# Performance work log

Measured on AMD Instinct MI355X. Metric: run time of the kernel, lower is better.

## Reference

```python
import jax, jax.numpy as jnp
import numpy as np

N, C_IN, C_OUT, T, V = 64, 128, 128, 128, 25
REL = C_IN // 8  # rel_channels = 16


def setup_inputs() -> dict:
    key = jax.random.key(0)
    ks = jax.random.split(key, 12)
    s_in = 1.0 / np.sqrt(C_IN)
    s_rel = 1.0 / np.sqrt(REL)
    return {
        "x": jax.random.normal(ks[0], (N, C_IN, T, V), jnp.float32),
        "A": jax.random.normal(ks[1], (V, V), jnp.float32),
        "alpha": jnp.float32(1.0),
        "W1": jax.random.normal(ks[2], (REL, C_IN), jnp.float32) * s_in,
        "b1": jnp.zeros((REL,), jnp.float32),
        "W2": jax.random.normal(ks[3], (REL, C_IN), jnp.float32) * s_in,
        "b2": jnp.zeros((REL,), jnp.float32),
        "W3": jax.random.normal(ks[4], (C_OUT, C_IN), jnp.float32) * s_in,
        "b3": jnp.zeros((C_OUT,), jnp.float32),
        "W4": jax.random.normal(ks[5], (C_OUT, REL), jnp.float32) * s_rel,
        "b4": jnp.zeros((C_OUT,), jnp.float32),
    }


def reference(x, A, alpha, W1, b1, W2, b2, W3, b3, W4, b4):
    # conv1(x).mean(-2) and conv2(x).mean(-2): 1x1 conv is linear, so mean over
    # T commutes with it -> compute mean first to avoid an (N,REL,T,V) temp.
    xm = x.mean(axis=2)                                        # (N, C, V)
    x1 = jnp.einsum('rc,ncv->nrv', W1, xm) + b1[None, :, None]  # (N, R, V)
    x2 = jnp.einsum('rc,ncv->nrv', W2, xm) + b2[None, :, None]  # (N, R, V)
    x3 = jnp.einsum('oc,nctv->notv', W3, x) + b3[None, :, None, None]  # (N,O,T,V)
    # tanh of broadcasted pairwise difference: (N, R, V, V)
    d = jnp.tanh(x1[:, :, :, None] - x2[:, :, None, :])
    # conv4 (1x1 over channel dim) -> learned per-channel adjacency
    adj = jnp.einsum('or,nrvu->novu', W4, d) + b4[None, :, None, None]
    adj = adj * alpha + A[None, None, :, :]                    # (N, O, V, V)
    return jnp.einsum('ncvu,nctv->nctu', adj, x3)              # (N, O, T, V)
```

## Files before the change

kernel.cpp:

```cpp
#include <hip/hip_runtime.h>


#define NB   64
#define CIN  128
#define COUT 128
#define TT   128
#define VV   25
#define REL  16

#define JT 25
#define KT 4
#define XF_BYTES (JT * KT * 1024)
#define X3_STRIDE 1040
#define LDS_BYTES (COUT * X3_STRIDE)

typedef __attribute__((ext_vector_type(8))) short bf16x8;
typedef __attribute__((ext_vector_type(4))) float f32x4;

__device__ inline short f2bf(float f) {
    unsigned u = __float_as_uint(f);
    u += 0x7fff + ((u >> 16) & 1);
    return (short)(u >> 16);
}

__launch_bounds__(256)
__global__ void k_mean(const float* __restrict__ x, float* __restrict__ xm) {
    __shared__ float tile[4 * 3200];
    int tid = threadIdx.x;
    int c0 = blockIdx.x * 4, n = blockIdx.y;
    const float* src = x + ((size_t)n * CIN + c0) * 3200;
    for (int i = tid; i < 3200; i += 256)
        *reinterpret_cast<float4*>(&tile[i * 4]) =
            *reinterpret_cast<const float4*>(src + (size_t)i * 4);
    __syncthreads();
    if (tid < 100) {
        int cl = tid / 25, v = tid - cl * 25;
        const float* r = &tile[cl * 3200 + v];
        float s = 0.f;
#pragma unroll
        for (int t = 0; t < TT; ++t) s += r[t * 25];
        xm[((size_t)n * CIN + c0 + cl) * 25 + v] = s * (1.0f / TT);
    }
}

__global__ void k_adj(const float* __restrict__ xm,
                      const float* __restrict__ A, const float* __restrict__ alphap,
                      const float* __restrict__ W1, const float* __restrict__ b1,
                      const float* __restrict__ W2, const float* __restrict__ b2,
                      const float* __restrict__ W4, const float* __restrict__ b4,
                      const float* __restrict__ W3, char* __restrict__ W3f,
                      char* __restrict__ adjT) {
    __shared__ char adjS[32 * 2048];
    __shared__ float xms[CIN * VV];
    __shared__ float W1s[REL * CIN];
    __shared__ float W2s[REL * CIN];
    __shared__ float x1s[REL * VV];
    __shared__ float x2s[REL * VV];
    __shared__ float W4s[32 * REL];
    __shared__ float b4s[32];

    int tid = threadIdx.x;
    int n = blockIdx.x;
    int o0 = blockIdx.y * 32;

    if (n == 0) {
#pragma unroll
        for (int pass = 0; pass < 2; ++pass) {
            int chunk = blockIdx.y * 512 + pass * 256 + tid;
            int l = chunk & 63;
            int frag = chunk >> 6;
            int ct = frag >> 2, kt = frag & 3;
            int c = ct * 16 + (l & 15);
            int kb = kt * 32 + 8 * (l >> 4);
            const float4 f0 = *reinterpret_cast<const float4*>(&W3[(size_t)c * CIN + kb]);
            const float4 f1 = *reinterpret_cast<const float4*>(&W3[(size_t)c * CIN + kb + 4]);
            bf16x8 vv;
            vv[0] = f2bf(f0.x); vv[1] = f2bf(f0.y); vv[2] = f2bf(f0.z); vv[3] = f2bf(f0.w);
            vv[4] = f2bf(f1.x); vv[5] = f2bf(f1.y); vv[6] = f2bf(f1.z); vv[7] = f2bf(f1.w);
            *reinterpret_cast<bf16x8*>(W3f + (size_t)chunk * 16) = vv;
        }
    }

    for (int i = tid; i < 16384; i += 256) reinterpret_cast<float*>(adjS)[i] = 0.f;
    for (int i = tid; i < CIN * VV; i += 256) xms[i] = xm[(size_t)n * CIN * VV + i];
    for (int i = tid; i < REL * CIN; i += 256) { W1s[i] = W1[i]; W2s[i] = W2[i]; }
    for (int i = tid; i < 32 * REL; i += 256) W4s[i] = W4[o0 * REL + i];
    if (tid < 32) b4s[tid] = b4[o0 + tid];
    __syncthreads();

    for (int task = tid; task < 2 * REL * VV; task += 256) {
        int rv = task % (REL * VV);
        int which = task / (REL * VV);
        int r = rv / VV, v = rv % VV;
        const float* Ws = which ? W2s : W1s;
        float s = 0.f;
#pragma unroll 8
        for (int c = 0; c < CIN; ++c) s = fmaf(Ws[r * CIN + c], xms[c * VV + v], s);
        s += which ? b2[r] : b1[r];
        (which ? x2s : x1s)[rv] = s;
    }
    __syncthreads();

    float alpha = alphap[0];
    for (int p = tid; p < VV * VV; p += 256) {
        int v = p / VV, u = p % VV;
        float d[REL];
#pragma unroll
        for (int r = 0; r < REL; ++r) d[r] = tanhf(x1s[r * VV + v] - x2s[r * VV + u]);
        float Avu = A[v * VV + u];
        int off = (u >> 4) * 1024 + (((u & 15) + 16 * (v >> 3)) * 16) + (v & 7) * 2;
        for (int oo = 0; oo < 32; ++oo) {
            float s = 0.f;
#pragma unroll
            for (int r = 0; r < REL; ++r) s = fmaf(W4s[oo * REL + r], d[r], s);
            float val = alpha * (s + b4s[oo]) + Avu;
            *(short*)(adjS + oo * 2048 + off) = f2bf(val);
        }
    }
    __syncthreads();

    float4* dst = reinterpret_cast<float4*>(adjT + (size_t)(n * COUT + o0) * 2048);
    const float4* src = reinterpret_cast<const float4*>(adjS);
    for (int i = tid; i < 4096; i += 256) dst[i] = src[i];
}

__launch_bounds__(1024)
__global__ void k_main(const float* __restrict__ x, const char* __restrict__ W3f,
                       const float* __restrict__ b3, const char* __restrict__ adjT,
                       float* __restrict__ out) {
    __shared__ __align__(16) char lds[LDS_BYTES];

    int tid = threadIdx.x;
    int tb = blockIdx.x, n = blockIdx.y;
    int lane = tid & 63, w = tid >> 6;
    int g = lane >> 4, lr = lane & 15;
    int ct = w >> 1, jh = w & 1;
    int jt0 = jh ? 13 : 0;
    int njt = jh ? 12 : 13;

    const float* xb = x + (size_t)n * (CIN * TT * VV) + tb * (16 * VV);

    bf16x8 xr[7];
#pragma unroll
    for (int q = 0; q < 7; ++q) {
        int chunk = tid + q * 1024;
        if (chunk < JT * KT * 64) {
            int l = chunk & 63;
            int frag = chunk >> 6;
            int kt = frag / JT, jt = frag % JT;
            int j = jt * 16 + (l & 15);
            int kb = kt * 32 + 8 * (l >> 4);
            const float* p = xb + (size_t)kb * (TT * VV) + j;
#pragma unroll
            for (int b = 0; b < 8; ++b) xr[q][b] = f2bf(p[(size_t)b * (TT * VV)]);
        }
    }
#pragma unroll
    for (int q = 0; q < 7; ++q) {
        int chunk = tid + q * 1024;
        if (chunk < JT * KT * 64)
            *reinterpret_cast<bf16x8*>(lds + (size_t)chunk * 16) = xr[q];
    }
    __syncthreads();

    f32x4 acc[13];
#pragma unroll
    for (int u = 0; u < 13; ++u) acc[u] = f32x4{0.f, 0.f, 0.f, 0.f};
#pragma unroll
    for (int kt = 0; kt < KT; ++kt) {
        bf16x8 a = *reinterpret_cast<const bf16x8*>(
            W3f + (size_t)((ct * 4 + kt) * 64 + lane) * 16);
#pragma unroll
        for (int u = 0; u < 13; ++u) {
            if (u < njt) {
                int jt = jt0 + u;
                bf16x8 bx = *reinterpret_cast<const bf16x8*>(
                    lds + (size_t)((kt * JT + jt) * 64 + lane) * 16);
                acc[u] = __builtin_amdgcn_mfma_f32_16x16x32_bf16(a, bx, acc[u], 0, 0, 0);
            }
        }
    }
    __syncthreads();

    int cbase = ct * 16 + 4 * g;
    float bv[4];
#pragma unroll
    for (int r = 0; r < 4; ++r) bv[r] = b3[cbase + r];
#pragma unroll
    for (int u = 0; u < 13; ++u) {
        if (u < njt) {
            int j = (jt0 + u) * 16 + lr;
            int t = j / 25, v = j - t * 25;
            int off = (t + 16 * (v >> 3)) * 16 + (v & 7) * 2;
#pragma unroll
            for (int r = 0; r < 4; ++r)
                *(short*)(lds + (size_t)(cbase + r) * X3_STRIDE + off) =
                    f2bf(acc[u][r] + bv[r]);
        }
    }
#pragma unroll
    for (int z = 0; z < 14; ++z) {
        int idx = tid + z * 1024;
        int c = idx / 112;
        int rem = idx - c * 112;
        int t = rem / 7, qq = rem - t * 7;
        *(short*)(lds + (size_t)c * X3_STRIDE + (t + 48) * 16 + 2 + qq * 2) = 0;
    }
    __syncthreads();

    const char* adjTb = adjT + (size_t)(n * COUT) * 2048;
    int t0 = tb * 16;
#pragma unroll
    for (int cc = 0; cc < 8; ++cc) {
        int c = w * 8 + cc;
        bf16x8 a = *reinterpret_cast<const bf16x8*>(lds + (size_t)c * X3_STRIDE + lane * 16);
        const bf16x8* bp = reinterpret_cast<const bf16x8*>(adjTb + (size_t)c * 2048);
        bf16x8 b0 = bp[lane];
        bf16x8 b1 = bp[64 + lane];
        f32x4 z = {0.f, 0.f, 0.f, 0.f};
        f32x4 d0 = __builtin_amdgcn_mfma_f32_16x16x32_bf16(a, b0, z, 0, 0, 0);
        f32x4 d1 = __builtin_amdgcn_mfma_f32_16x16x32_bf16(a, b1, z, 0, 0, 0);
        float* ob = out + ((size_t)(n * COUT + c) * TT + t0) * VV;
#pragma unroll
        for (int rr = 0; rr < 4; ++rr) {
            int t = 4 * g + rr;
            ob[(size_t)t * VV + lr] = d0[rr];
            if (lr < 9) ob[(size_t)t * VV + 16 + lr] = d1[rr];
        }
    }
}

extern "C" void kernel_launch(void* const* d_in, const int* in_sizes, int n_in,
                              void* d_out, int out_size, void* d_ws, size_t ws_size,
                              hipStream_t stream) {
    const float* x     = (const float*)d_in[0];
    const float* A     = (const float*)d_in[1];
    const float* alpha = (const float*)d_in[2];
    const float* W1    = (const float*)d_in[3];
    const float* b1    = (const float*)d_in[4];
    const float* W2    = (const float*)d_in[5];
    const float* b2    = (const float*)d_in[6];
    const float* W3    = (const float*)d_in[7];
    const float* b3    = (const float*)d_in[8];
    const float* W4    = (const float*)d_in[9];
    const float* b4    = (const float*)d_in[10];
    float* out = (float*)d_out;

    float* xm  = (float*)d_ws;
    char* adjT = (char*)d_ws + 819200;
    char* W3f  = (char*)d_ws + 819200 + 16777216;

    k_mean<<<dim3(CIN / 4, NB), 256, 0, stream>>>(x, xm);
    k_adj<<<dim3(NB, 4), 256, 0, stream>>>(xm, A, alpha, W1, b1, W2, b2, W4, b4,
                                           W3, W3f, adjT);
    k_main<<<dim3(TT / 16, NB), 1024, 0, stream>>>(x, W3f, b3, adjT, out);
}
```

Baseline: 115.4 us.

## Fuse mean with bf16 fragment packing of x in prep kernel

Result: slower. 162.3 us (+40.7%).

```diff
diff --git a/kernel.cpp b/kernel.cpp
--- a/kernel.cpp
+++ b/kernel.cpp
@@ -24,22 +24,80 @@
 }
 
 __launch_bounds__(256)
-__global__ void k_mean(const float* __restrict__ x, float* __restrict__ xm) {
-    __shared__ float tile[4 * 3200];
+__global__ void k_prep(const float* __restrict__ x, float* __restrict__ xm,
+                       char* __restrict__ Xf) {
+    __shared__ float tile[32 * 400];
     int tid = threadIdx.x;
-    int c0 = blockIdx.x * 4, n = blockIdx.y;
-    const float* src = x + ((size_t)n * CIN + c0) * 3200;
-    for (int i = tid; i < 3200; i += 256)
-        *reinterpret_cast<float4*>(&tile[i * 4]) =
-            *reinterpret_cast<const float4*>(src + (size_t)i * 4);
-    __syncthreads();
-    if (tid < 100) {
-        int cl = tid / 25, v = tid - cl * 25;
-        const float* r = &tile[cl * 3200 + v];
-        float s = 0.f;
-#pragma unroll
-        for (int t = 0; t < TT; ++t) s += r[t * 25];
-        xm[((size_t)n * CIN + c0 + cl) * 25 + v] = s * (1.0f / TT);
+    int kt = blockIdx.x, n = blockIdx.y;
+    int c0 = kt * 32;
+    float msum0 = 0.f, msum1 = 0.f, msum2 = 0.f, msum3 = 0.f;
+
+    for (int tb = 0; tb < 8; ++tb) {
+        __syncthreads();
+        const float* src = x + (((size_t)n * CIN + c0) * TT + tb * 16) * VV;
+        for (int i = tid; i < 3200; i += 256) {
+            int c = i / 100, q = i - c * 100;
+            *reinterpret_cast<float4*>(&tile[c * 400 + q * 4]) =
+                *reinterpret_cast<const float4*>(src + (size_t)c * (TT * VV) + q * 4);
+        }
+        __syncthreads();
+        {
+            int p = tid;
+            {   int c = p / 25, v = p - c * 25;
+                const float* r = &tile[c * 400 + v];
+                float s = 0.f;
+#pragma unroll
+                for (int t = 0; t < 16; ++t) s += r[t * 25];
+                msum0 += s; }
+            p = tid + 256;
+            {   int c = p / 25, v = p - c * 25;
+                const float* r = &tile[c * 400 + v];
+                float s = 0.f;
+#pragma unroll
+                for (int t = 0; t < 16; ++t) s += r[t * 25];
+                msum1 += s; }
+            p = tid + 512;
+            {   int c = p / 25, v = p - c * 25;
+                const float* r = &tile[c * 400 + v];
+                float s = 0.f;
+#pragma unroll
+                for (int t = 0; t < 16; ++t) s += r[t * 25];
+                msum2 += s; }
+            p = tid + 768;
+            if (p < 800) {
+                int c = p / 25, v = p - c * 25;
+                const float* r = &tile[c * 400 + v];
+                float s = 0.f;
+#pragma unroll
+                for (int t = 0; t < 16; ++t) s += r[t * 25];
+                msum3 += s; }
+        }
+        char* dst = Xf + (size_t)(n * 8 + tb) * XF_BYTES + (size_t)kt * 25 * 1024;
+        for (int ch = tid; ch < 1600; ch += 256) {
+            int l = ch & 63, jt = ch >> 6;
+            int j = jt * 16 + (l & 15);
+            int cl = 8 * (l >> 4);
+            bf16x8 v;
+#pragma unroll
+            for (int b = 0; b < 8; ++b) v[b] = f2bf(tile[(cl + b) * 400 + j]);
+            *reinterpret_cast<bf16x8*>(dst + (size_t)ch * 16) = v;
+        }
+    }
+    {
+        int p = tid;
+        { int c = p / 25, v = p - c * 25;
+          xm[((size_t)n * CIN + c0 + c) * VV + v] = msum0 * (1.0f / TT); }
+        p = tid + 256;
+        { int c = p / 25, v = p - c * 25;
+          xm[((size_t)n * CIN + c0 + c) * VV + v] = msum1 * (1.0f / TT); }
+        p = tid + 512;
+        { int c = p / 25, v = p - c * 25;
+          xm[((size_t)n * CIN + c0 + c) * VV + v] = msum2 * (1.0f / TT); }
+        p = tid + 768;
+        if (p < 800) {
+            int c = p / 25, v = p - c * 25;
+            xm[((size_t)n * CIN + c0 + c) * VV + v] = msum3 * (1.0f / TT);
+        }
     }
 }
 
@@ -125,7 +183,7 @@
 }
 
 __launch_bounds__(1024)
-__global__ void k_main(const float* __restrict__ x, const char* __restrict__ W3f,
+__global__ void k_main(const char* __restrict__ Xf, const char* __restrict__ W3f,
                        const float* __restrict__ b3, const char* __restrict__ adjT,
                        float* __restrict__ out) {
     __shared__ __align__(16) char lds[LDS_BYTES];
@@ -138,28 +196,13 @@
     int jt0 = jh ? 13 : 0;
     int njt = jh ? 12 : 13;
 
-    const float* xb = x + (size_t)n * (CIN * TT * VV) + tb * (16 * VV);
-
-    bf16x8 xr[7];
-#pragma unroll
-    for (int q = 0; q < 7; ++q) {
-        int chunk = tid + q * 1024;
-        if (chunk < JT * KT * 64) {
-            int l = chunk & 63;
-            int frag = chunk >> 6;
-            int kt = frag / JT, jt = frag % JT;
-            int j = jt * 16 + (l & 15);
-            int kb = kt * 32 + 8 * (l >> 4);
-            const float* p = xb + (size_t)kb * (TT * VV) + j;
-#pragma unroll
-            for (int b = 0; b < 8; ++b) xr[q][b] = f2bf(p[(size_t)b * (TT * VV)]);
-        }
-    }
+    const char* xfb = Xf + (size_t)(n * 8 + tb) * XF_BYTES;
 #pragma unroll
     for (int q = 0; q < 7; ++q) {
         int chunk = tid + q * 1024;
         if (chunk < JT * KT * 64)
-            *reinterpret_cast<bf16x8*>(lds + (size_t)chunk * 16) = xr[q];
+            *reinterpret_cast<bf16x8*>(lds + (size_t)chunk * 16) =
+                *reinterpret_cast<const bf16x8*>(xfb + (size_t)chunk * 16);
     }
     __syncthreads();
 
@@ -249,9 +292,10 @@
     float* xm  = (float*)d_ws;
     char* adjT = (char*)d_ws + 819200;
     char* W3f  = (char*)d_ws + 819200 + 16777216;
-
-    k_mean<<<dim3(CIN / 4, NB), 256, 0, stream>>>(x, xm);
+    char* Xf   = (char*)d_ws + 819200 + 16777216 + 32768;
+
+    k_prep<<<dim3(KT, NB), 256, 0, stream>>>(x, xm, Xf);
     k_adj<<<dim3(NB, 4), 256, 0, stream>>>(xm, A, alpha, W1, b1, W2, b2, W4, b4,
                                            W3, W3f, adjT);
-    k_main<<<dim3(TT / 16, NB), 1024, 0, stream>>>(x, W3f, b3, adjT, out);
-}
+    k_main<<<dim3(TT / 16, NB), 1024, 0, stream>>>(Xf, W3f, b3, adjT, out);
+}
```

## Fuse mean pass with bf16 fragment-layout pre-packing of x for main kernel

Applied to the files above, without the earlier changes.

New measurement: 124.8 us. 1.08x slower.

```diff
diff --git a/kernel.cpp b/kernel.cpp
--- a/kernel.cpp
+++ b/kernel.cpp
@@ -13,6 +13,7 @@
 #define XF_BYTES (JT * KT * 1024)
 #define X3_STRIDE 1040
 #define LDS_BYTES (COUT * X3_STRIDE)
+#define TSTRIDE 416
 
 typedef __attribute__((ext_vector_type(8))) short bf16x8;
 typedef __attribute__((ext_vector_type(4))) float f32x4;
@@ -24,22 +25,50 @@
 }
 
 __launch_bounds__(256)
-__global__ void k_mean(const float* __restrict__ x, float* __restrict__ xm) {
-    __shared__ float tile[4 * 3200];
+__global__ void k_prep(const float* __restrict__ x, float* __restrict__ xm,
+                       char* __restrict__ Xf) {
+    __shared__ float tile[32 * TSTRIDE];
     int tid = threadIdx.x;
-    int c0 = blockIdx.x * 4, n = blockIdx.y;
-    const float* src = x + ((size_t)n * CIN + c0) * 3200;
-    for (int i = tid; i < 3200; i += 256)
-        *reinterpret_cast<float4*>(&tile[i * 4]) =
-            *reinterpret_cast<const float4*>(src + (size_t)i * 4);
-    __syncthreads();
-    if (tid < 100) {
-        int cl = tid / 25, v = tid - cl * 25;
-        const float* r = &tile[cl * 3200 + v];
-        float s = 0.f;
-#pragma unroll
-        for (int t = 0; t < TT; ++t) s += r[t * 25];
-        xm[((size_t)n * CIN + c0 + cl) * 25 + v] = s * (1.0f / TT);
+    int kt = blockIdx.x >> 3, tb = blockIdx.x & 7, n = blockIdx.y;
+    int c0 = kt * 32;
+
+    const float* src = x + (size_t)(n * CIN + c0) * 3200 + tb * 400;
+#pragma unroll
+    for (int p = 0; p < 13; ++p) {
+        int i = tid + p * 256;
+        if (i < 3200) {
+            int c = i / 100, q = i - c * 100;
+            int sw = ((c >> 3) & 1) << 4;
+            *reinterpret_cast<float4*>(&tile[c * TSTRIDE + ((q * 4) ^ sw)]) =
+                *reinterpret_cast<const float4*>(src + (size_t)c * 3200 + q * 4);
+        }
+    }
+    __syncthreads();
+
+#pragma unroll
+    for (int pp = 0; pp < 4; ++pp) {
+        int p = tid + pp * 256;
+        if (p < 800) {
+            int c = p / 25, v = p - c * 25;
+            int sw = ((c >> 3) & 1) << 4;
+            float s = 0.f;
+#pragma unroll
+            for (int t = 0; t < 16; ++t) s += tile[c * TSTRIDE + ((t * 25 + v) ^ sw)];
+            atomicAdd(&xm[((size_t)n * CIN + c0 + c) * VV + v], s * (1.0f / TT));
+        }
+    }
+
+    char* dst = Xf + (size_t)(n * 8 + tb) * XF_BYTES + (size_t)kt * 25600;
+    for (int ch = tid; ch < 1600; ch += 256) {
+        int l = ch & 63, jt = ch >> 6;
+        int j = jt * 16 + (l & 15);
+        int cl = 8 * (l >> 4);
+        int sw = ((l >> 4) & 1) << 4;
+        bf16x8 v;
+#pragma unroll
+        for (int b = 0; b < 8; ++b)
+            v[b] = f2bf(tile[(cl + b) * TSTRIDE + (j ^ sw)]);
+        *reinterpret_cast<bf16x8*>(dst + (size_t)ch * 16) = v;
     }
 }
 
@@ -125,7 +154,7 @@
 }
 
 __launch_bounds__(1024)
-__global__ void k_main(const float* __restrict__ x, const char* __restrict__ W3f,
+__global__ void k_main(const char* __restrict__ Xf, const char* __restrict__ W3f,
                        const float* __restrict__ b3, const char* __restrict__ adjT,
                        float* __restrict__ out) {
     __shared__ __align__(16) char lds[LDS_BYTES];
@@ -138,28 +167,13 @@
     int jt0 = jh ? 13 : 0;
     int njt = jh ? 12 : 13;
 
-    const float* xb = x + (size_t)n * (CIN * TT * VV) + tb * (16 * VV);
-
-    bf16x8 xr[7];
-#pragma unroll
-    for (int q = 0; q < 7; ++q) {
-        int chunk = tid + q * 1024;
-        if (chunk < JT * KT * 64) {
-            int l = chunk & 63;
-            int frag = chunk >> 6;
-            int kt = frag / JT, jt = frag % JT;
-            int j = jt * 16 + (l & 15);
-            int kb = kt * 32 + 8 * (l >> 4);
-            const float* p = xb + (size_t)kb * (TT * VV) + j;
-#pragma unroll
-            for (int b = 0; b < 8; ++b) xr[q][b] = f2bf(p[(size_t)b * (TT * VV)]);
-        }
-    }
+    const char* xfb = Xf + (size_t)(n * 8 + tb) * XF_BYTES;
 #pragma unroll
     for (int q = 0; q < 7; ++q) {
         int chunk = tid + q * 1024;
         if (chunk < JT * KT * 64)
-            *reinterpret_cast<bf16x8*>(lds + (size_t)chunk * 16) = xr[q];
+            *reinterpret_cast<bf16x8*>(lds + (size_t)chunk * 16) =
+                *reinterpret_cast<const bf16x8*>(xfb + (size_t)chunk * 16);
     }
     __syncthreads();
 
@@ -249,9 +263,11 @@
     float* xm  = (float*)d_ws;
     char* adjT = (char*)d_ws + 819200;
     char* W3f  = (char*)d_ws + 819200 + 16777216;
-
-    k_mean<<<dim3(CIN / 4, NB), 256, 0, stream>>>(x, xm);
+    char* Xf   = (char*)d_ws + 819200 + 16777216 + 32768;
+
+    hipMemsetAsync(xm, 0, 819200, stream);
+    k_prep<<<dim3(32, NB), 256, 0, stream>>>(x, xm, Xf);
     k_adj<<<dim3(NB, 4), 256, 0, stream>>>(xm, A, alpha, W1, b1, W2, b2, W4, b4,
                                            W3, W3f, adjT);
-    k_main<<<dim3(TT / 16, NB), 1024, 0, stream>>>(x, W3f, b3, adjT, out);
-}
+    k_main<<<dim3(TT / 16, NB), 1024, 0, stream>>>(Xf, W3f, b3, adjT, out);
+}
```
